# Optimization experiments

Measured on AMD Instinct MI355X. Metric: run time of the kernel, lower is better.

Reference implementation:

```python
import jax, jax.numpy as jnp
import numpy as np

N, K, E = 262144, 8, 16
DT = 0.02  # config.delta_time


def _mono(x, w1, b1, w2, b2):
    # monotonic_fun with increasing=False: out_linear(exp(-in_linear(x)))
    return jnp.exp(-(x @ w1.T + b1)) @ w2.T + b2


def _isin(a, b):
    # rowwise torch.isin: a [N,P], b [N,Q] -> [N,P] bool
    return (a[:, :, None] == b[:, None, :]).any(-1)


def _angle_clamp(vec, v, ang):
    # torch.cosine_similarity(v, vec, dim=-1).abs() > ang gate (eps=1e-8)
    num = jnp.einsum('nd,nrd->nr', v, vec)
    den = jnp.maximum(jnp.linalg.norm(v, axis=-1)[:, None] * jnp.linalg.norm(vec, axis=-1), 1e-8)
    keep = jnp.abs(num / den) > ang
    return jnp.where(keep[..., None], vec, 0.0)


def _linear_params(key, fan_in, fan_out):
    a = 1.0 / np.sqrt(fan_in)
    k1, k2 = jax.random.split(key)
    # weightConstraint(min_b=0) clamps weights to >= 0 at init
    w = jnp.maximum(jax.random.uniform(k1, (fan_out, fan_in), minval=-a, maxval=a), 0.0)
    b = jax.random.uniform(k2, (fan_out,), minval=-a, maxval=a)
    return w, b


def _mono_params(key):
    k1, k2 = jax.random.split(key)
    w1, b1 = _linear_params(k1, 1, E)
    w2, b2 = _linear_params(k2, E, 1)
    return w1, b1, w2, b2


def setup_inputs() -> dict:
    key = jax.random.key(0)
    ks = jax.random.split(key, 12)
    ego = jax.random.normal(ks[0], (N, 16), dtype=jnp.float32)
    ego = ego.at[:, 0].set(jnp.arange(N, dtype=jnp.float32))
    # surrounding-vehicle id columns 7..14 as small integer ids (floats)
    ego = ego.at[:, 7:15].set(jax.random.randint(ks[1], (N, 8), 0, 21).astype(jnp.float32))
    nei = jax.random.normal(ks[2], (N, K, 16), dtype=jnp.float32)
    nei = nei.at[:, :, 0].set(jax.random.randint(ks[3], (N, K), 1, 21).astype(jnp.float32))
    border = jax.random.uniform(ks[4], (4,), dtype=jnp.float32) * 10.0 + 1.0
    recording_time = jnp.zeros((N, K, 2), dtype=jnp.float32)
    p_dest = jax.random.uniform(ks[5], (2,), dtype=jnp.float32)  # relu(rand(2))
    angle = jax.nn.sigmoid(jax.random.uniform(ks[6], (1,), dtype=jnp.float32))
    d = {'ego': ego, 'nei': nei, 'border': border, 'recording_time': recording_time,
         'p_dest': p_dest, 'angle': angle}
    for name, kk in (('rep', ks[7]), ('att', ks[8]), ('bor', ks[9]), ('del', ks[10])):
        w1, b1, w2, b2 = _mono_params(kk)
        d[name + '_w1'], d[name + '_b1'], d[name + '_w2'], d[name + '_b2'] = w1, b1, w2, b2
    return d


def reference(ego, nei, border, recording_time, p_dest, angle,
              rep_w1, rep_b1, rep_w2, rep_b2,
              att_w1, att_b1, att_w2, att_b2,
              bor_w1, bor_b1, bor_w2, bor_b2,
              del_w1, del_b1, del_w2, del_b2):
    ang = angle[0]
    v = ego[:, 3:5]                                        # ego velocity [N,2]
    speed = jnp.linalg.norm(v, axis=-1)
    desired = jnp.stack([speed, jnp.zeros_like(speed)], axis=1)
    f_dest = ((p_dest[1] * desired - v) / p_dest[0])[:, None, :]   # [N,1,2]

    nei_id = nei[:, :, 0]                                  # [N,K]
    idx = _isin(nei_id, ego[:, 7:15]) & (nei_id != 0)

    # --- recording_time buffer update (vectorized remain/new/pad concat) ---
    buf_id, buf_ct = recording_time[:, :, 0], recording_time[:, :, 1]
    ifin = _isin(buf_id, nei_id)                           # buffer slots still present
    ct2 = buf_ct + ifin.astype(buf_ct.dtype)               # increment their counts
    ifnew = (~_isin(nei_id, buf_id)) & (nei_id != 0)       # brand-new neighbor ids
    cand = jnp.concatenate([jnp.stack([buf_id, ct2], -1),
                            jnp.stack([nei_id, jnp.ones_like(nei_id)], -1)], axis=1)  # [N,2K,2]
    ar = jnp.arange(K)
    BIG = 1 << 20
    keyord = jnp.concatenate([jnp.where(ifin, ar, BIG), jnp.where(ifnew, ar + K, BIG)], axis=1)
    order = jnp.argsort(keyord, axis=1)[:, :K]             # stable: remain order, then new, then pad
    skey = jnp.take_along_axis(keyord, order, axis=1)
    new_buf = jnp.where((skey < BIG)[..., None],
                        jnp.take_along_axis(cand, order[..., None], axis=1), 1.0)  # pad with ones
    count = new_buf[:, :, 1]                               # [N,K]

    # --- neighbor attraction / repulsion ---
    r = jnp.where(idx[..., None], nei[:, :, 1:3] - ego[:, None, 1:3], 0.0)
    rn = jnp.linalg.norm(r, axis=-1)
    rns = jnp.where(idx, rn, 1.0)                          # safe divisor (masked slots zeroed below)
    dirn = r / rns[..., None]
    f_attr = (_mono(count[..., None], del_w1, del_b1, del_w2, del_b2)
              * _mono(rn[..., None], att_w1, att_b1, att_w2, att_b2) * dirn)
    v_nei = nei[:, :, 3:5]
    b = rn + jnp.sum((r + v_nei * DT) ** 2, -1) - jnp.sum((v_nei * DT) ** 2, -1)
    b = jnp.sqrt(jnp.maximum(jnp.where(idx, b, 1.0), 1e-12)) / 2.0
    f_repu = _mono(b[..., None], rep_w1, rep_b1, rep_w2, rep_b2) * dirn
    f_attr = jnp.where(idx[..., None], f_attr, 0.0)
    f_repu = jnp.where(idx[..., None], f_repu, 0.0)

    # --- border repulsion (y-axis only), select_lane = [0, -1] ---
    rb_all = ego[:, 2:3] - border                          # [N,4]
    rb = jnp.stack([rb_all[:, 0], rb_all[:, -1]], axis=1)  # [N,2]
    rbn = jnp.abs(rb)
    f_by = _mono(rbn[..., None], bor_w1, bor_b1, bor_w2, bor_b2) * (rb / rbn)[..., None]
    f_bor = jnp.concatenate([jnp.zeros_like(f_by), f_by], axis=-1)  # [N,2,2]

    f_destination = _angle_clamp(f_dest, v, ang).sum(1)
    f_neighbors = _angle_clamp(f_attr, v, ang).sum(1) + _angle_clamp(f_repu, v, ang).sum(1)
    f_border = _angle_clamp(f_bor, v, ang).sum(1)
    return jnp.stack([f_destination, f_neighbors, f_border], axis=1)  # [N,3,2]
```

## Files before the change

kernel.cpp:

```cpp
#include <hip/hip_runtime.h>
#include <math.h>

#define EN 16

__device__ __forceinline__ float mono_fast(float x,
    const float* __restrict__ w1, const float* __restrict__ b1,
    const float* __restrict__ w2, const float* __restrict__ b2) {
    float acc = 0.0f;
#pragma unroll
    for (int e = 0; e < EN; ++e) {
        float pre = fmaf(x, w1[e], b1[e]);
        acc = fmaf(__expf(-pre), w2[e], acc);
    }
    return acc + b2[0];
}

extern "C" __global__ void __launch_bounds__(256)
sfm_kernel(const float* __restrict__ ego, const float* __restrict__ nei,
           const float* __restrict__ border, const float* __restrict__ rec,
           const float* __restrict__ p_dest, const float* __restrict__ angle,
           const float* __restrict__ rep_w1, const float* __restrict__ rep_b1,
           const float* __restrict__ rep_w2, const float* __restrict__ rep_b2,
           const float* __restrict__ att_w1, const float* __restrict__ att_b1,
           const float* __restrict__ att_w2, const float* __restrict__ att_b2,
           const float* __restrict__ bor_w1, const float* __restrict__ bor_b1,
           const float* __restrict__ bor_w2, const float* __restrict__ bor_b2,
           const float* __restrict__ del_w1, const float* __restrict__ del_b1,
           const float* __restrict__ del_w2, const float* __restrict__ del_b2,
           float* __restrict__ out, int N)
{
    const int gid = blockIdx.x * blockDim.x + threadIdx.x;
    const int n = gid >> 3;
    const int k = gid & 7;
    if (n >= N) return;
    const int lane = threadIdx.x & 63;
    const int gbase = lane & ~7;

    const float ang = angle[0];
    const float p0 = p_dest[0], p1 = p_dest[1];

    const float* er = ego + (size_t)n * 16;
    float4 ea = *(const float4*)(er);
    float4 eb = *(const float4*)(er + 4);
    float4 ec = *(const float4*)(er + 8);
    float4 ed = *(const float4*)(er + 12);
    const float px = ea.y, py = ea.z, vx = ea.w, vy = eb.x;
    const float speed = sqrtf(vx * vx + vy * vy);

    const float* nb = nei + (size_t)n * 128 + (size_t)k * 16;
    float4 na = *(const float4*)nb;
    const float nvyv = nb[4];
    const float nid = na.x;

    float2 rc = *(const float2*)(rec + (size_t)n * 16 + (size_t)k * 2);
    const float bid = rc.x, bct = rc.y;

    bool fin = (bid == nid);
#pragma unroll
    for (int t = 1; t < 8; ++t)
        fin = fin || (bid == __shfl_xor(nid, t));

    unsigned long long bal = __ballot(fin);
    unsigned finM = (unsigned)((bal >> gbase) & 0xFFull);
    int popcFin = __popc(finM);
    int jsel = 0, cbits = 0;
#pragma unroll
    for (int j = 0; j < 8; ++j) {
        int bit = (finM >> j) & 1;
        if (bit && cbits == k) jsel = j;
        cbits += bit;
    }
    float bctj = __shfl(bct, gbase + jsel);
    float cntk = (k < popcFin) ? (bctj + 1.0f) : 1.0f;

    bool match = (nid == eb.w) || (nid == ec.x) || (nid == ec.y) || (nid == ec.z)
              || (nid == ec.w) || (nid == ed.x) || (nid == ed.y) || (nid == ed.z);
    const bool idxk = match && (nid != 0.0f);

    float rx = idxk ? (na.y - px) : 0.0f;
    float ry = idxk ? (na.z - py) : 0.0f;
    float rn = sqrtf(rx * rx + ry * ry);
    float rns = idxk ? rn : 1.0f;
    float dx = rx / rns, dy = ry / rns;

    float att = mono_fast(rn,   att_w1, att_b1, att_w2, att_b2);
    float del = mono_fast(cntk, del_w1, del_b1, del_w2, del_b2);
    float sa = del * att;
    float fax = idxk ? sa * dx : 0.0f;
    float fay = idxk ? sa * dy : 0.0f;

    float nbx = 0.0f, nby = 0.0f;
    {
        float num = vx * fax + vy * fay;
        float fn = sqrtf(fax * fax + fay * fay);
        float den = fmaxf(speed * fn, 1e-8f);
        if (fabsf(num / den) > ang) { nbx += fax; nby += fay; }
    }

    float sxv = na.w * 0.02f, syv = nvyv * 0.02f;
    float ox = rx + sxv, oy = ry + syv;
    float bsum = rn + (ox * ox + oy * oy) - (sxv * sxv + syv * syv);
    float bgate = idxk ? bsum : 1.0f;
    float bb = sqrtf(fmaxf(bgate, 1e-12f)) * 0.5f;
    float rep = mono_fast(bb, rep_w1, rep_b1, rep_w2, rep_b2);
    float frx = idxk ? rep * dx : 0.0f;
    float fry = idxk ? rep * dy : 0.0f;
    {
        float num = vx * frx + vy * fry;
        float fn = sqrtf(frx * frx + fry * fry);
        float den = fmaxf(speed * fn, 1e-8f);
        if (fabsf(num / den) > ang) { nbx += frx; nby += fry; }
    }

    float bsel = (k == 0) ? border[0] : border[3];
    float rb = py - bsel;
    float rbn = fabsf(rb);
    float mb = mono_fast(rbn, bor_w1, bor_b1, bor_w2, bor_b2);
    float fby = mb * (rb / rbn);
    float bory = 0.0f;
    {
        float num = vy * fby;
        float den = fmaxf(speed * fabsf(fby), 1e-8f);
        if ((fabsf(num / den) > ang) && (k < 2)) bory = fby;
    }

#pragma unroll
    for (int m = 1; m < 8; m <<= 1) {
        nbx  += __shfl_xor(nbx,  m);
        nby  += __shfl_xor(nby,  m);
        bory += __shfl_xor(bory, m);
    }

    float fdx = (p1 * speed - vx) / p0;
    float fdy = (0.0f - vy) / p0;
    float fdex = 0.0f, fdey = 0.0f;
    {
        float num = vx * fdx + vy * fdy;
        float fn = sqrtf(fdx * fdx + fdy * fdy);
        float den = fmaxf(speed * fn, 1e-8f);
        if (fabsf(num / den) > ang) { fdex = fdx; fdey = fdy; }
    }

    float wv = (k == 0) ? fdex
             : (k == 1) ? fdey
             : (k == 2) ? nbx
             : (k == 3) ? nby
             : (k == 4) ? 0.0f
             : bory;
    if (k < 6) out[(size_t)n * 6 + k] = wv;
}

extern "C" void kernel_launch(void* const* d_in, const int* in_sizes, int n_in,
                              void* d_out, int out_size, void* d_ws, size_t ws_size,
                              hipStream_t stream) {
    const float* ego    = (const float*)d_in[0];
    const float* nei    = (const float*)d_in[1];
    const float* border = (const float*)d_in[2];
    const float* rec    = (const float*)d_in[3];
    const float* p_dest = (const float*)d_in[4];
    const float* angle  = (const float*)d_in[5];
    const float* rep_w1 = (const float*)d_in[6];
    const float* rep_b1 = (const float*)d_in[7];
    const float* rep_w2 = (const float*)d_in[8];
    const float* rep_b2 = (const float*)d_in[9];
    const float* att_w1 = (const float*)d_in[10];
    const float* att_b1 = (const float*)d_in[11];
    const float* att_w2 = (const float*)d_in[12];
    const float* att_b2 = (const float*)d_in[13];
    const float* bor_w1 = (const float*)d_in[14];
    const float* bor_b1 = (const float*)d_in[15];
    const float* bor_w2 = (const float*)d_in[16];
    const float* bor_b2 = (const float*)d_in[17];
    const float* del_w1 = (const float*)d_in[18];
    const float* del_b1 = (const float*)d_in[19];
    const float* del_w2 = (const float*)d_in[20];
    const float* del_b2 = (const float*)d_in[21];
    float* out = (float*)d_out;

    int N = in_sizes[0] / 16;
    long long threads = (long long)N * 8;
    dim3 grid((unsigned)((threads + 255) / 256));
    sfm_kernel<<<grid, 256, 0, stream>>>(
        ego, nei, border, rec, p_dest, angle,
        rep_w1, rep_b1, rep_w2, rep_b2,
        att_w1, att_b1, att_w2, att_b2,
        bor_w1, bor_b1, bor_w2, bor_b2,
        del_w1, del_b1, del_w2, del_b2,
        out, N);
}
```

Before: 251.5 us.

## Stage MLP weights in LDS, precompute constant del, skip redundant work

Loads the four monotonic-MLP weight sets into shared memory as packed float4 with pre-negated inputs. A single thread evaluates the del network at count 1 once per block. A wavefront ballot skips the isin/shuffle count logic when no recording ids are nonzero. The del MLP is evaluated only when the count differs from 1, and the border MLP only on the lanes that use it. This aims to cut exp and ALU work per thread, at the cost of block-level syncs and LDS traffic.

```diff
diff --git a/kernel.cpp b/kernel.cpp
--- a/kernel.cpp
+++ b/kernel.cpp
@@ -2,18 +2,6 @@
 #include <math.h>
 
 #define EN 16
-
-__device__ __forceinline__ float mono_fast(float x,
-    const float* __restrict__ w1, const float* __restrict__ b1,
-    const float* __restrict__ w2, const float* __restrict__ b2) {
-    float acc = 0.0f;
-#pragma unroll
-    for (int e = 0; e < EN; ++e) {
-        float pre = fmaf(x, w1[e], b1[e]);
-        acc = fmaf(__expf(-pre), w2[e], acc);
-    }
-    return acc + b2[0];
-}
 
 extern "C" __global__ void __launch_bounds__(256)
 sfm_kernel(const float* __restrict__ ego, const float* __restrict__ nei,
@@ -29,6 +17,35 @@
            const float* __restrict__ del_w2, const float* __restrict__ del_b2,
            float* __restrict__ out, int N)
 {
+    __shared__ float4 wlds[64];
+    __shared__ float sconst[8];
+
+    {
+        const int t = threadIdx.x;
+        if (t < 64) {
+            const int net = t >> 4, e = t & 15;
+            const float* w1p = (net == 0) ? att_w1 : (net == 1) ? rep_w1 : (net == 2) ? del_w1 : bor_w1;
+            const float* b1p = (net == 0) ? att_b1 : (net == 1) ? rep_b1 : (net == 2) ? del_b1 : bor_b1;
+            const float* w2p = (net == 0) ? att_w2 : (net == 1) ? rep_w2 : (net == 2) ? del_w2 : bor_w2;
+            wlds[t] = make_float4(-w1p[e], -b1p[e], w2p[e], 0.0f);
+        } else if (t < 68) {
+            const int net = t - 64;
+            const float* b2p = (net == 0) ? att_b2 : (net == 1) ? rep_b2 : (net == 2) ? del_b2 : bor_b2;
+            sconst[net] = b2p[0];
+        }
+        __syncthreads();
+        if (t == 0) {
+            float acc = 0.0f;
+#pragma unroll
+            for (int e = 0; e < EN; ++e) {
+                float4 w = wlds[32 + e];
+                acc = fmaf(__expf(w.x + w.y), w.z, acc);
+            }
+            sconst[4] = acc + sconst[2];
+        }
+        __syncthreads();
+    }
+
     const int gid = blockIdx.x * blockDim.x + threadIdx.x;
     const int n = gid >> 3;
     const int k = gid & 7;
@@ -55,23 +72,29 @@
     float2 rc = *(const float2*)(rec + (size_t)n * 16 + (size_t)k * 2);
     const float bid = rc.x, bct = rc.y;
 
-    bool fin = (bid == nid);
-#pragma unroll
-    for (int t = 1; t < 8; ++t)
-        fin = fin || (bid == __shfl_xor(nid, t));
-
-    unsigned long long bal = __ballot(fin);
-    unsigned finM = (unsigned)((bal >> gbase) & 0xFFull);
-    int popcFin = __popc(finM);
-    int jsel = 0, cbits = 0;
-#pragma unroll
-    for (int j = 0; j < 8; ++j) {
-        int bit = (finM >> j) & 1;
-        if (bit && cbits == k) jsel = j;
-        cbits += bit;
-    }
-    float bctj = __shfl(bct, gbase + jsel);
-    float cntk = (k < popcFin) ? (bctj + 1.0f) : 1.0f;
+    unsigned long long m1 = __ballot(bid != 0.0f);
+    unsigned long long m2 = __ballot(nid == 0.0f);
+    float cntk;
+    if ((m1 | m2) == 0ull) {
+        cntk = 1.0f;
+    } else {
+        bool fin = (bid == nid);
+#pragma unroll
+        for (int t = 1; t < 8; ++t)
+            fin = fin || (bid == __shfl_xor(nid, t));
+        unsigned long long bal = __ballot(fin);
+        unsigned finM = (unsigned)((bal >> gbase) & 0xFFull);
+        int popcFin = __popc(finM);
+        int jsel = 0, cbits = 0;
+#pragma unroll
+        for (int j = 0; j < 8; ++j) {
+            int bit = (finM >> j) & 1;
+            if (bit && cbits == k) jsel = j;
+            cbits += bit;
+        }
+        float bctj = __shfl(bct, gbase + jsel);
+        cntk = (k < popcFin) ? (bctj + 1.0f) : 1.0f;
+    }
 
     bool match = (nid == eb.w) || (nid == ec.x) || (nid == ec.y) || (nid == ec.z)
               || (nid == ec.w) || (nid == ed.x) || (nid == ed.y) || (nid == ed.z);
@@ -83,45 +106,71 @@
     float rns = idxk ? rn : 1.0f;
     float dx = rx / rns, dy = ry / rns;
 
-    float att = mono_fast(rn,   att_w1, att_b1, att_w2, att_b2);
-    float del = mono_fast(cntk, del_w1, del_b1, del_w2, del_b2);
-    float sa = del * att;
-    float fax = idxk ? sa * dx : 0.0f;
-    float fay = idxk ? sa * dy : 0.0f;
-
-    float nbx = 0.0f, nby = 0.0f;
-    {
-        float num = vx * fax + vy * fay;
-        float fn = sqrtf(fax * fax + fay * fay);
-        float den = fmaxf(speed * fn, 1e-8f);
-        if (fabsf(num / den) > ang) { nbx += fax; nby += fay; }
-    }
-
     float sxv = na.w * 0.02f, syv = nvyv * 0.02f;
     float ox = rx + sxv, oy = ry + syv;
     float bsum = rn + (ox * ox + oy * oy) - (sxv * sxv + syv * syv);
     float bgate = idxk ? bsum : 1.0f;
     float bb = sqrtf(fmaxf(bgate, 1e-12f)) * 0.5f;
-    float rep = mono_fast(bb, rep_w1, rep_b1, rep_w2, rep_b2);
-    float frx = idxk ? rep * dx : 0.0f;
-    float fry = idxk ? rep * dy : 0.0f;
-    {
+
+    float acca = 0.0f, accr = 0.0f;
+#pragma unroll
+    for (int e = 0; e < EN; ++e) {
+        float4 wa = wlds[e];
+        float4 wr = wlds[16 + e];
+        acca = fmaf(__expf(fmaf(rn, wa.x, wa.y)), wa.z, acca);
+        accr = fmaf(__expf(fmaf(bb, wr.x, wr.y)), wr.z, accr);
+    }
+    float att = acca + sconst[0];
+    float rep = accr + sconst[1];
+
+    float del;
+    if (cntk == 1.0f) {
+        del = sconst[4];
+    } else {
+        float accd = 0.0f;
+#pragma unroll
+        for (int e = 0; e < EN; ++e) {
+            float4 wd = wlds[32 + e];
+            accd = fmaf(__expf(fmaf(cntk, wd.x, wd.y)), wd.z, accd);
+        }
+        del = accd + sconst[2];
+    }
+
+    float nbx = 0.0f, nby = 0.0f;
+    {
+        float sa = del * att;
+        float fax = idxk ? sa * dx : 0.0f;
+        float fay = idxk ? sa * dy : 0.0f;
+        float num = vx * fax + vy * fay;
+        float fn = sqrtf(fax * fax + fay * fay);
+        float den = fmaxf(speed * fn, 1e-8f);
+        if (fabsf(num / den) > ang) { nbx += fax; nby += fay; }
+    }
+    {
+        float frx = idxk ? rep * dx : 0.0f;
+        float fry = idxk ? rep * dy : 0.0f;
         float num = vx * frx + vy * fry;
         float fn = sqrtf(frx * frx + fry * fry);
         float den = fmaxf(speed * fn, 1e-8f);
         if (fabsf(num / den) > ang) { nbx += frx; nby += fry; }
     }
 
-    float bsel = (k == 0) ? border[0] : border[3];
-    float rb = py - bsel;
-    float rbn = fabsf(rb);
-    float mb = mono_fast(rbn, bor_w1, bor_b1, bor_w2, bor_b2);
-    float fby = mb * (rb / rbn);
     float bory = 0.0f;
-    {
+    if (k < 2) {
+        float bsel = (k == 0) ? border[0] : border[3];
+        float rb = py - bsel;
+        float rbn = fabsf(rb);
+        float accb = 0.0f;
+#pragma unroll
+        for (int e = 0; e < EN; ++e) {
+            float4 wb = wlds[48 + e];
+            accb = fmaf(__expf(fmaf(rbn, wb.x, wb.y)), wb.z, accb);
+        }
+        float mb = accb + sconst[3];
+        float fby = mb * (rb / rbn);
         float num = vy * fby;
         float den = fmaxf(speed * fabsf(fby), 1e-8f);
-        if ((fabsf(num / den) > ang) && (k < 2)) bory = fby;
+        if (fabsf(num / den) > ang) bory = fby;
     }
 
 #pragma unroll
```

Result: slower. 259.1 us (+3.0%).
